# Performance work log

Hardware: AMD Instinct MI355X
Metric: run time of the kernel (lower is better)

Reference implementation:

```python
import jax, jax.numpy as jnp
import numpy as np

N = 50000
E = 600000
IN_C = 128
HID_C = 128
OUT_C = 128


def _glorot(key, shape):
    fan_in, fan_out = shape[0], shape[1]
    lim = np.sqrt(6.0 / (fan_in + fan_out))
    return jax.random.uniform(key, shape, jnp.float32, -lim, lim)


def setup_inputs() -> dict:
    key = jax.random.key(0)
    ks = jax.random.split(key, 10)
    x = jax.random.normal(ks[0], (N, IN_C), jnp.float32)
    edge_index = jax.random.randint(ks[1], (2, E), 0, N, jnp.int64)
    return {
        "x": x,
        "edge_index": edge_index,
        # SAGEConv1: lin_l (aggregated, with bias) and lin_r (root, no bias)
        "W1_l": _glorot(ks[2], (IN_C, HID_C)),
        "b1_l": jnp.zeros((HID_C,), jnp.float32),
        "W1_r": _glorot(ks[3], (IN_C, HID_C)),
        # SAGEConv2
        "W2_l": _glorot(ks[4], (HID_C, OUT_C)),
        "b2_l": jnp.zeros((OUT_C,), jnp.float32),
        "W2_r": _glorot(ks[5], (HID_C, OUT_C)),
        # final Linear(hidden+out -> out)
        "W_lin": _glorot(ks[6], (HID_C + OUT_C, OUT_C)),
        "b_lin": jnp.zeros((OUT_C,), jnp.float32),
    }


def _sage_conv(x, src, dst, W_l, b_l, W_r):
    # mean-aggregate source features onto destination nodes
    msg = x[src]                                   # [E, C] gather
    agg = jax.ops.segment_sum(msg, dst, num_segments=N)        # [N, C]
    cnt = jax.ops.segment_sum(jnp.ones((src.shape[0],), x.dtype), dst,
                              num_segments=N)                   # [N]
    mean = agg / jnp.maximum(cnt, 1.0)[:, None]
    return mean @ W_l + b_l + x @ W_r


def reference(x, edge_index, W1_l, b1_l, W1_r, W2_l, b2_l, W2_r, W_lin, b_lin):
    src, dst = edge_index[0], edge_index[1]
    x1 = jax.nn.relu(_sage_conv(x, src, dst, W1_l, b1_l, W1_r))   # [N, HID]
    x2 = jax.nn.relu(_sage_conv(x1, src, dst, W2_l, b2_l, W2_r))  # [N, OUT]
    return jnp.concatenate([x1, x2], axis=-1) @ W_lin + b_lin     # [N, OUT]
```

## Files before the change

kernel.cpp:

```cpp
#include <hip/hip_runtime.h>


typedef _Float16 f16;
typedef unsigned int u32;
typedef __attribute__((ext_vector_type(4))) _Float16 f16x4;
typedef __attribute__((ext_vector_type(8))) _Float16 f16x8;
typedef __attribute__((ext_vector_type(4))) float f32x4;

#define RNB 128

__global__ void prep_kernel(const float* __restrict__ x, f16* __restrict__ xh, int n4,
                            const int* __restrict__ ei, int* __restrict__ ghist, int E,
                            const float* __restrict__ W1l, const float* __restrict__ W1r,
                            const float* __restrict__ W2l, const float* __restrict__ W2r,
                            const float* __restrict__ Wlin, f16* __restrict__ wt,
                            int cb, int wb) {
  int b = blockIdx.x;
  if (b < cb) {
    int i = b * 256 + threadIdx.x;
    if (i < n4) {
      const float4 v = ((const float4*)x)[i];
      f16x4 h = { (f16)v.x, (f16)v.y, (f16)v.z, (f16)v.w };
      ((f16x4*)xh)[i] = h;
    }
  } else if (b < cb + wb) {
    int tid = (b - cb) * 256 + threadIdx.x;
    int w = tid >> 15, idx = tid & 32767;
    int j = idx & 7, n = (idx >> 3) & 127, chunk = idx >> 10;
    int k = chunk * 8 + j;
    float v;
    if (w == 0) v = (k < 128) ? W1l[k * 128 + n] : W1r[(k - 128) * 128 + n];
    else if (w == 1) v = (k < 128) ? W2l[k * 128 + n] : W2r[(k - 128) * 128 + n];
    else v = Wlin[k * 128 + n];
    wt[tid] = (f16)v;
  } else {
    __shared__ int h[256];
    int tid = threadIdx.x, rb = b - cb - wb;
    h[tid] = 0;
    __syncthreads();
    int per = (E + RNB - 1) / RNB;
    int s = rb * per, e = s + per; if (e > E) e = E;
    for (int i = s + tid; i < e; i += 256) atomicAdd(&h[ei[E + i] >> 8], 1);
    __syncthreads();
    ghist[tid * RNB + rb] = h[tid];
  }
}

__device__ inline int block_excl_scan256(int v, int* ws) {
  int lane = threadIdx.x & 63, w = threadIdx.x >> 6;
  int incl = v;
#pragma unroll
  for (int o = 1; o < 64; o <<= 1) {
    int u = __shfl_up(incl, o);
    if (lane >= o) incl += u;
  }
  if (lane == 63) ws[w] = incl;
  __syncthreads();
  int base = 0;
#pragma unroll
  for (int i = 0; i < 4; ++i) base += (i < w) ? ws[i] : 0;
  return base + incl - v;
}

__global__ void radix_scatter(const int* __restrict__ ei, const int* __restrict__ ghist,
                              u32* __restrict__ tmp, int E) {
  __shared__ int cur[256];
  __shared__ int ws[4];
  int tid = threadIdx.x, b = blockIdx.x;
  const int* row = ghist + tid * RNB;
  int part = 0, rest = 0;
  for (int i = 0; i < b; ++i) part += row[i];
  for (int i = b; i < RNB; ++i) rest += row[i];
  int total = part + rest;
  int excl = block_excl_scan256(total, ws);
  cur[tid] = excl + part;
  __syncthreads();
  int per = (E + RNB - 1) / RNB;
  int s = b * per, e = s + per; if (e > E) e = E;
  for (int i = s + tid; i < e; i += 256) {
    int d = ei[E + i], sr = ei[i];
    int pos = atomicAdd(&cur[d >> 8], 1);
    tmp[pos] = ((u32)sr << 8) | (u32)(d & 255);
  }
}

__global__ void radix_bucket(const u32* __restrict__ tmp, const int* __restrict__ ghist,
                             int* __restrict__ srcs, int* __restrict__ off,
                             int N, int E, int HB) {
  __shared__ int h[256], sc[256], cur[256];
  __shared__ int bsc[257];
  __shared__ int ws[4];
  int tid = threadIdx.x, hb = blockIdx.x;
  const int* row = ghist + tid * RNB;
  int total = 0;
#pragma unroll 4
  for (int i = 0; i < RNB; ++i) total += row[i];
  int excl = block_excl_scan256(total, ws);
  bsc[tid] = excl;
  if (tid == 255) bsc[256] = E;
  h[tid] = 0;
  __syncthreads();
  int start = bsc[hb];
  int end = bsc[hb + 1];
  for (int i = start + tid; i < end; i += 256) atomicAdd(&h[tmp[i] & 255u], 1);
  __syncthreads();
  sc[tid] = h[tid];
  __syncthreads();
  for (int o = 1; o < 256; o <<= 1) {
    int u = (tid >= o) ? sc[tid - o] : 0;
    __syncthreads();
    sc[tid] += u;
    __syncthreads();
  }
  int exclb = sc[tid] - h[tid];
  int v = (hb << 8) + tid;
  if (v < N) off[v] = start + exclb;
  if (hb == 0 && tid == 0) off[N] = E;
  cur[tid] = start + exclb;
  __syncthreads();
  for (int i = start + tid; i < end; i += 256) {
    u32 p = tmp[i];
    int pos = atomicAdd(&cur[p & 255u], 1);
    srcs[pos] = (int)(p >> 8);
  }
}

#define AGG_R 6
__global__ void aggregate_kernel(const f16* __restrict__ feat, const int* __restrict__ off,
                                 const int* __restrict__ srcs, f16* __restrict__ meanf, int n) {
  int pair = (int)((blockIdx.x * blockDim.x + threadIdx.x) >> 6);
  int w0 = pair * 2;
  if (w0 >= n) return;
  int w1 = w0 + 1;
  int lane = threadIdx.x & 63;
  int sub = lane >> 4, n15 = lane & 15;
  int beg0 = off[w0], end0 = off[w0 + 1];
  int beg1 = end0;
  int end1 = (w1 < n) ? off[w1 + 1] : end0;
  int deg0 = end0 - beg0, deg1 = end1 - beg1;

  int s0[AGG_R], s1[AGG_R];
  bool v0[AGG_R], v1[AGG_R];
#pragma unroll
  for (int k = 0; k < AGG_R; ++k) {
    int p = 4 * k + sub;
    v0[k] = p < deg0;  s0[k] = v0[k] ? srcs[beg0 + p] : 0;
    v1[k] = p < deg1;  s1[k] = v1[k] ? srcs[beg1 + p] : 0;
  }
  f16x8 g0[AGG_R], g1[AGG_R];
#pragma unroll
  for (int k = 0; k < AGG_R; ++k) {
    if (v0[k]) g0[k] = *(const f16x8*)(feat + (size_t)s0[k] * 128 + n15 * 8);
    if (v1[k]) g1[k] = *(const f16x8*)(feat + (size_t)s1[k] * 128 + n15 * 8);
  }
  float acc0[8] = {}, acc1[8] = {};
#pragma unroll
  for (int k = 0; k < AGG_R; ++k) {
    if (v0[k]) {
#pragma unroll
      for (int j = 0; j < 8; ++j) acc0[j] += (float)g0[k][j];
    }
    if (v1[k]) {
#pragma unroll
      for (int j = 0; j < 8; ++j) acc1[j] += (float)g1[k][j];
    }
  }
  for (int e = beg0 + 4 * AGG_R; e < end0; e += 4) {
    if (sub < end0 - e) {
      int s = srcs[e + sub];
      f16x8 g = *(const f16x8*)(feat + (size_t)s * 128 + n15 * 8);
#pragma unroll
      for (int j = 0; j < 8; ++j) acc0[j] += (float)g[j];
    }
  }
  for (int e = beg1 + 4 * AGG_R; e < end1; e += 4) {
    if (sub < end1 - e) {
      int s = srcs[e + sub];
      f16x8 g = *(const f16x8*)(feat + (size_t)s * 128 + n15 * 8);
#pragma unroll
      for (int j = 0; j < 8; ++j) acc1[j] += (float)g[j];
    }
  }
#pragma unroll
  for (int j = 0; j < 8; ++j) {
    acc0[j] += __shfl_xor(acc0[j], 16);
    acc0[j] += __shfl_xor(acc0[j], 32);
    acc1[j] += __shfl_xor(acc1[j], 16);
    acc1[j] += __shfl_xor(acc1[j], 32);
  }
  if (sub == 0) {
    float inv = 1.0f / fmaxf((float)deg0, 1.0f);
    f16x8 o;
#pragma unroll
    for (int j = 0; j < 8; ++j) o[j] = (f16)(acc0[j] * inv);
    *(f16x8*)(meanf + (size_t)w0 * 128 + n15 * 8) = o;
  } else if (sub == 1 && w1 < n) {
    float inv = 1.0f / fmaxf((float)deg1, 1.0f);
    f16x8 o;
#pragma unroll
    for (int j = 0; j < 8; ++j) o[j] = (f16)(acc1[j] * inv);
    *(f16x8*)(meanf + (size_t)w1 * 128 + n15 * 8) = o;
  }
}

template <bool RELU, bool OUT16>
__global__ __launch_bounds__(256, 2) void gemm_kernel(
    const f16* __restrict__ U, const f16* __restrict__ V, const f16* __restrict__ Wt,
    const float* __restrict__ bias, void* __restrict__ outp, int M) {
  __shared__ f16 ldsb[32768];
  int tid = threadIdx.x;
  int wave = tid >> 6, lane = tid & 63;
  int quad = lane >> 4, n15 = lane & 15;
  int m0 = blockIdx.x * 128 + wave * 32;
  int kq = quad * 8;

  f16x8 a[2][8];
#pragma unroll
  for (int r = 0; r < 2; ++r) {
    int row = m0 + r * 16 + n15;
    int rowc = row < M ? row : M - 1;
    const f16* bu = U + (size_t)rowc * 128 + kq;
    const f16* bv = V + (size_t)rowc * 128 + kq;
#pragma unroll
    for (int kk = 0; kk < 4; ++kk) a[r][kk] = *(const f16x8*)(bu + kk * 32);
#pragma unroll
    for (int kk = 4; kk < 8; ++kk) a[r][kk] = *(const f16x8*)(bv + (kk - 4) * 32);
  }

#pragma unroll
  for (int it = 0; it < 16; ++it) {
    int idx = it * 256 + tid;
    ((f16x8*)ldsb)[idx] = ((const f16x8*)Wt)[idx];
  }
  __syncthreads();

  f32x4 acc[2][8] = {};
#pragma unroll
  for (int kk = 0; kk < 8; ++kk) {
#pragma unroll
    for (int t = 0; t < 8; ++t) {
      f16x8 b = ((const f16x8*)ldsb)[(kk * 4 + quad) * 128 + t * 16 + n15];
#pragma unroll
      for (int r = 0; r < 2; ++r)
        acc[r][t] = __builtin_amdgcn_mfma_f32_16x16x32_f16(a[r][kk], b, acc[r][t], 0, 0, 0);
    }
  }

  int rbase0 = m0 + quad * 4;
#pragma unroll
  for (int t = 0; t < 8; ++t) {
    float bv = bias[t * 16 + n15];
#pragma unroll
    for (int r = 0; r < 2; ++r) {
#pragma unroll
      for (int i = 0; i < 4; ++i) {
        int row = rbase0 + r * 16 + i;
        if (row < M) {
          float v = acc[r][t][i] + bv;
          if (RELU) v = fmaxf(v, 0.f);
          size_t idx = (size_t)row * 128 + t * 16 + n15;
          if (OUT16) ((f16*)outp)[idx] = (f16)v;
          else       ((float*)outp)[idx] = v;
        }
      }
    }
  }
}

__global__ __launch_bounds__(256, 2) void gemm23_kernel(
    const f16* __restrict__ U,
    const f16* __restrict__ V,
    const f16* __restrict__ Wt2, const f16* __restrict__ Wt3,
    const float* __restrict__ b2, const float* __restrict__ b3,
    float* __restrict__ out, int M) {
  __shared__ f16 ldsb[32768];
  int tid = threadIdx.x;
  int wave = tid >> 6, lane = tid & 63;
  int quad = lane >> 4, n15 = lane & 15;
  int m0 = blockIdx.x * 128 + wave * 32;
  int kq = quad * 8;

  f16x8 a[2][8];
#pragma unroll
  for (int r = 0; r < 2; ++r) {
    int row = m0 + r * 16 + n15;
    int rowc = row < M ? row : M - 1;
    const f16* bu = U + (size_t)rowc * 128 + kq;
    const f16* bv = V + (size_t)rowc * 128 + kq;
#pragma unroll
    for (int kk = 0; kk < 4; ++kk) a[r][kk] = *(const f16x8*)(bu + kk * 32);
#pragma unroll
    for (int kk = 4; kk < 8; ++kk) a[r][kk] = *(const f16x8*)(bv + (kk - 4) * 32);
  }

#pragma unroll
  for (int it = 0; it < 16; ++it) {
    int idx = it * 256 + tid;
    ((f16x8*)ldsb)[idx] = ((const f16x8*)Wt2)[idx];
  }
  __syncthreads();

  f32x4 acc[2][8] = {};
#pragma unroll
  for (int kk = 0; kk < 8; ++kk) {
#pragma unroll
    for (int t = 0; t < 8; ++t) {
      f16x8 b = ((const f16x8*)ldsb)[(kk * 4 + quad) * 128 + t * 16 + n15];
#pragma unroll
      for (int r = 0; r < 2; ++r)
        acc[r][t] = __builtin_amdgcn_mfma_f32_16x16x32_f16(a[r][kk], b, acc[r][t], 0, 0, 0);
    }
  }

  __syncthreads();

#pragma unroll
  for (int t = 0; t < 8; ++t) {
    float bv = b2[t * 16 + n15];
    int chunk = t * 2 + (n15 >> 3);
    int offc = n15 & 7;
#pragma unroll
    for (int r = 0; r < 2; ++r) {
#pragma unroll
      for (int i = 0; i < 4; ++i) {
        int rowl = wave * 32 + r * 16 + quad * 4 + i;
        float v = fmaxf(acc[r][t][i] + bv, 0.f);
        ldsb[rowl * 128 + (((chunk ^ (rowl & 15)) << 3) | offc)] = (f16)v;
      }
    }
  }
  __syncthreads();

  f16x8 a2[2][4];
#pragma unroll
  for (int r = 0; r < 2; ++r) {
    int rowl = wave * 32 + r * 16 + n15;
#pragma unroll
    for (int kk2 = 0; kk2 < 4; ++kk2) {
      int chunk = kk2 * 4 + quad;
      a2[r][kk2] = *(const f16x8*)(ldsb + rowl * 128 + ((chunk ^ (rowl & 15)) << 3));
    }
  }

  f32x4 acc3[2][8] = {};
#pragma unroll
  for (int kk = 0; kk < 8; ++kk) {
#pragma unroll
    for (int t = 0; t < 8; ++t) {
      f16x8 b = ((const f16x8*)Wt3)[(kk * 4 + quad) * 128 + t * 16 + n15];
#pragma unroll
      for (int r = 0; r < 2; ++r) {
        f16x8 av = (kk < 4) ? a[r][4 + kk] : a2[r][kk - 4];
        acc3[r][t] = __builtin_amdgcn_mfma_f32_16x16x32_f16(av, b, acc3[r][t], 0, 0, 0);
      }
    }
  }

  int rbase0 = m0 + quad * 4;
#pragma unroll
  for (int t = 0; t < 8; ++t) {
    float bv = b3[t * 16 + n15];
#pragma unroll
    for (int r = 0; r < 2; ++r) {
#pragma unroll
      for (int i = 0; i < 4; ++i) {
        int row = rbase0 + r * 16 + i;
        if (row < M)
          out[(size_t)row * 128 + t * 16 + n15] = acc3[r][t][i] + bv;
      }
    }
  }
}

extern "C" void kernel_launch(void* const* d_in, const int* in_sizes, int n_in,
                              void* d_out, int out_size, void* d_ws, size_t ws_size,
                              hipStream_t stream) {
  (void)n_in; (void)out_size; (void)ws_size;
  const float* x    = (const float*)d_in[0];
  const int*   ei   = (const int*)d_in[1];
  const float* W1l  = (const float*)d_in[2];
  const float* b1l  = (const float*)d_in[3];
  const float* W1r  = (const float*)d_in[4];
  const float* W2l  = (const float*)d_in[5];
  const float* b2l  = (const float*)d_in[6];
  const float* W2r  = (const float*)d_in[7];
  const float* Wlin = (const float*)d_in[8];
  const float* blin = (const float*)d_in[9];
  const int N = in_sizes[0] / 128;
  const int E = in_sizes[1] / 2;

  char* ws = (char*)d_ws;
  size_t o = 0;
  auto alloc = [&](size_t bytes) {
    char* p = ws + o;
    o = (o + bytes + 255) & ~(size_t)255;
    return p;
  };
  f16*  xh   = (f16*)alloc((size_t)N * 128 * 2);
  f16*  x1h  = (f16*)alloc((size_t)N * 128 * 2);
  f16*  mh   = (f16*)alloc((size_t)N * 128 * 2);
  f16*  wt   = (f16*)alloc((size_t)3 * 32768 * 2);
  int*  off  = (int*)alloc(((size_t)N + 1) * 4);
  int*  srcs = (int*)alloc((size_t)E * 4);
  u32*  tmp  = (u32*)alloc((size_t)E * 4);
  int*  ghist= (int*)alloc(256 * RNB * 4);
  f16* wt1 = wt, *wt2 = wt + 32768, *wt3 = wt + 65536;

  const int n4 = N * 128 / 4;
  const int cb = (n4 + 255) / 256;
  const int wb = (3 * 32768) / 256;
  const int HB = (N + 255) / 256;

  prep_kernel<<<cb + wb + RNB, 256, 0, stream>>>(x, xh, n4, ei, ghist, E,
                                                 W1l, W1r, W2l, W2r, Wlin, wt, cb, wb);
  radix_scatter<<<RNB, 256, 0, stream>>>(ei, ghist, tmp, E);
  radix_bucket<<<HB, 256, 0, stream>>>(tmp, ghist, srcs, off, N, E, HB);

  const int aggBlocks  = ((N + 1) / 2 + 3) / 4;
  const int gemmBlocks = (N + 127) / 128;

  aggregate_kernel<<<aggBlocks, 256, 0, stream>>>(xh, off, srcs, mh, N);
  gemm_kernel<true, true><<<gemmBlocks, 256, 0, stream>>>(mh, xh, wt1, b1l, x1h, N);
  aggregate_kernel<<<aggBlocks, 256, 0, stream>>>(x1h, off, srcs, mh, N);
  gemm23_kernel<<<gemmBlocks, 256, 0, stream>>>(mh, x1h, wt2, wt3, b2l, blin,
                                                (float*)d_out, N);
}
```

Before: 229.0 us.

## Fuse mean aggregation with SAGE linear layers into per-tile kernels

Replaces the separate aggregate and GEMM kernels with one kernel per layer. Each block aggregates 32 nodes' neighbor means into LDS and immediately runs the MFMA GEMM with weights streamed through LDS in quarter chunks. This removes the global round-trip of the mean buffer and two launches. In exchange the row tiles are smaller, there are extra barriers for weight chunk reloads, and each block reloads the full weight matrices, i.e. more weight traffic per row.

Measured after the change: 226.1 us. Within noise of the previous version (-1.3%).

```diff
diff --git a/kernel.cpp b/kernel.cpp
--- a/kernel.cpp
+++ b/kernel.cpp
@@ -126,247 +126,198 @@
 }
 
 #define AGG_R 6
-__global__ void aggregate_kernel(const f16* __restrict__ feat, const int* __restrict__ off,
-                                 const int* __restrict__ srcs, f16* __restrict__ meanf, int n) {
-  int pair = (int)((blockIdx.x * blockDim.x + threadIdx.x) >> 6);
-  int w0 = pair * 2;
-  if (w0 >= n) return;
-  int w1 = w0 + 1;
-  int lane = threadIdx.x & 63;
-  int sub = lane >> 4, n15 = lane & 15;
-  int beg0 = off[w0], end0 = off[w0 + 1];
-  int beg1 = end0;
-  int end1 = (w1 < n) ? off[w1 + 1] : end0;
-  int deg0 = end0 - beg0, deg1 = end1 - beg1;
-
-  int s0[AGG_R], s1[AGG_R];
-  bool v0[AGG_R], v1[AGG_R];
-#pragma unroll
-  for (int k = 0; k < AGG_R; ++k) {
-    int p = 4 * k + sub;
-    v0[k] = p < deg0;  s0[k] = v0[k] ? srcs[beg0 + p] : 0;
-    v1[k] = p < deg1;  s1[k] = v1[k] ? srcs[beg1 + p] : 0;
-  }
-  f16x8 g0[AGG_R], g1[AGG_R];
-#pragma unroll
-  for (int k = 0; k < AGG_R; ++k) {
-    if (v0[k]) g0[k] = *(const f16x8*)(feat + (size_t)s0[k] * 128 + n15 * 8);
-    if (v1[k]) g1[k] = *(const f16x8*)(feat + (size_t)s1[k] * 128 + n15 * 8);
-  }
-  float acc0[8] = {}, acc1[8] = {};
-#pragma unroll
-  for (int k = 0; k < AGG_R; ++k) {
-    if (v0[k]) {
-#pragma unroll
-      for (int j = 0; j < 8; ++j) acc0[j] += (float)g0[k][j];
-    }
-    if (v1[k]) {
-#pragma unroll
-      for (int j = 0; j < 8; ++j) acc1[j] += (float)g1[k][j];
-    }
-  }
-  for (int e = beg0 + 4 * AGG_R; e < end0; e += 4) {
-    if (sub < end0 - e) {
-      int s = srcs[e + sub];
-      f16x8 g = *(const f16x8*)(feat + (size_t)s * 128 + n15 * 8);
-#pragma unroll
-      for (int j = 0; j < 8; ++j) acc0[j] += (float)g[j];
-    }
-  }
-  for (int e = beg1 + 4 * AGG_R; e < end1; e += 4) {
-    if (sub < end1 - e) {
-      int s = srcs[e + sub];
-      f16x8 g = *(const f16x8*)(feat + (size_t)s * 128 + n15 * 8);
-#pragma unroll
-      for (int j = 0; j < 8; ++j) acc1[j] += (float)g[j];
-    }
-  }
-#pragma unroll
-  for (int j = 0; j < 8; ++j) {
-    acc0[j] += __shfl_xor(acc0[j], 16);
-    acc0[j] += __shfl_xor(acc0[j], 32);
-    acc1[j] += __shfl_xor(acc1[j], 16);
-    acc1[j] += __shfl_xor(acc1[j], 32);
-  }
-  if (sub == 0) {
-    float inv = 1.0f / fmaxf((float)deg0, 1.0f);
-    f16x8 o;
-#pragma unroll
-    for (int j = 0; j < 8; ++j) o[j] = (f16)(acc0[j] * inv);
-    *(f16x8*)(meanf + (size_t)w0 * 128 + n15 * 8) = o;
-  } else if (sub == 1 && w1 < n) {
-    float inv = 1.0f / fmaxf((float)deg1, 1.0f);
-    f16x8 o;
-#pragma unroll
-    for (int j = 0; j < 8; ++j) o[j] = (f16)(acc1[j] * inv);
-    *(f16x8*)(meanf + (size_t)w1 * 128 + n15 * 8) = o;
-  }
-}
-
-template <bool RELU, bool OUT16>
-__global__ __launch_bounds__(256, 2) void gemm_kernel(
-    const f16* __restrict__ U, const f16* __restrict__ V, const f16* __restrict__ Wt,
-    const float* __restrict__ bias, void* __restrict__ outp, int M) {
-  __shared__ f16 ldsb[32768];
+template <bool HEAD>
+__global__ __launch_bounds__(256, 4) void fused_kernel(
+    const f16* __restrict__ feat,
+    const int* __restrict__ off, const int* __restrict__ srcs,
+    const f16* __restrict__ WtA, const f16* __restrict__ WtB,
+    const float* __restrict__ bA, const float* __restrict__ bB,
+    void* __restrict__ outp, int n) {
+  __shared__ f16 lds[16384];
   int tid = threadIdx.x;
   int wave = tid >> 6, lane = tid & 63;
-  int quad = lane >> 4, n15 = lane & 15;
-  int m0 = blockIdx.x * 128 + wave * 32;
-  int kq = quad * 8;
-
-  f16x8 a[2][8];
-#pragma unroll
-  for (int r = 0; r < 2; ++r) {
-    int row = m0 + r * 16 + n15;
-    int rowc = row < M ? row : M - 1;
-    const f16* bu = U + (size_t)rowc * 128 + kq;
-    const f16* bv = V + (size_t)rowc * 128 + kq;
-#pragma unroll
-    for (int kk = 0; kk < 4; ++kk) a[r][kk] = *(const f16x8*)(bu + kk * 32);
-#pragma unroll
-    for (int kk = 4; kk < 8; ++kk) a[r][kk] = *(const f16x8*)(bv + (kk - 4) * 32);
-  }
-
-#pragma unroll
-  for (int it = 0; it < 16; ++it) {
-    int idx = it * 256 + tid;
-    ((f16x8*)ldsb)[idx] = ((const f16x8*)Wt)[idx];
-  }
-  __syncthreads();
-
-  f32x4 acc[2][8] = {};
-#pragma unroll
-  for (int kk = 0; kk < 8; ++kk) {
-#pragma unroll
-    for (int t = 0; t < 8; ++t) {
-      f16x8 b = ((const f16x8*)ldsb)[(kk * 4 + quad) * 128 + t * 16 + n15];
-#pragma unroll
-      for (int r = 0; r < 2; ++r)
-        acc[r][t] = __builtin_amdgcn_mfma_f32_16x16x32_f16(a[r][kk], b, acc[r][t], 0, 0, 0);
-    }
-  }
-
-  int rbase0 = m0 + quad * 4;
-#pragma unroll
-  for (int t = 0; t < 8; ++t) {
-    float bv = bias[t * 16 + n15];
-#pragma unroll
-    for (int r = 0; r < 2; ++r) {
+  int sub = lane >> 4, n15 = lane & 15;
+  int base = blockIdx.x * 32;
+
+#pragma unroll
+  for (int i = 0; i < 4; ++i)
+    ((f16x8*)lds)[i * 256 + tid] = ((const f16x8*)WtA)[i * 256 + tid];
+
+#pragma unroll 1
+  for (int p = 0; p < 4; ++p) {
+    int ln0 = p * 8 + wave * 2;
+    int w0 = base + ln0, w1 = w0 + 1;
+    bool a0 = w0 < n, a1 = w1 < n;
+    int beg0 = a0 ? off[w0] : 0;
+    int end0 = a0 ? off[w0 + 1] : 0;
+    int beg1 = end0;
+    int end1 = a1 ? off[w1 + 1] : end0;
+    int deg0 = end0 - beg0, deg1 = end1 - beg1;
+
+    int s0[AGG_R], s1[AGG_R];
+    bool v0[AGG_R], v1[AGG_R];
+#pragma unroll
+    for (int k = 0; k < AGG_R; ++k) {
+      int pp = 4 * k + sub;
+      v0[k] = pp < deg0;  s0[k] = v0[k] ? srcs[beg0 + pp] : 0;
+      v1[k] = pp < deg1;  s1[k] = v1[k] ? srcs[beg1 + pp] : 0;
+    }
+    f16x8 g0[AGG_R], g1[AGG_R];
+#pragma unroll
+    for (int k = 0; k < AGG_R; ++k) {
+      if (v0[k]) g0[k] = *(const f16x8*)(feat + (size_t)s0[k] * 128 + n15 * 8);
+      if (v1[k]) g1[k] = *(const f16x8*)(feat + (size_t)s1[k] * 128 + n15 * 8);
+    }
+    float acc0[8] = {}, acc1[8] = {};
+#pragma unroll
+    for (int k = 0; k < AGG_R; ++k) {
+      if (v0[k]) {
+#pragma unroll
+        for (int j = 0; j < 8; ++j) acc0[j] += (float)g0[k][j];
+      }
+      if (v1[k]) {
+#pragma unroll
+        for (int j = 0; j < 8; ++j) acc1[j] += (float)g1[k][j];
+      }
+    }
+    for (int e = beg0 + 4 * AGG_R; e < end0; e += 4) {
+      if (sub < end0 - e) {
+        int s = srcs[e + sub];
+        f16x8 g = *(const f16x8*)(feat + (size_t)s * 128 + n15 * 8);
+#pragma unroll
+        for (int j = 0; j < 8; ++j) acc0[j] += (float)g[j];
+      }
+    }
+    for (int e = beg1 + 4 * AGG_R; e < end1; e += 4) {
+      if (sub < end1 - e) {
+        int s = srcs[e + sub];
+        f16x8 g = *(const f16x8*)(feat + (size_t)s * 128 + n15 * 8);
+#pragma unroll
+        for (int j = 0; j < 8; ++j) acc1[j] += (float)g[j];
+      }
+    }
+#pragma unroll
+    for (int j = 0; j < 8; ++j) {
+      acc0[j] += __shfl_xor(acc0[j], 16);
+      acc0[j] += __shfl_xor(acc0[j], 32);
+      acc1[j] += __shfl_xor(acc1[j], 16);
+      acc1[j] += __shfl_xor(acc1[j], 32);
+    }
+    if (sub == 0) {
+      float inv = 1.0f / fmaxf((float)deg0, 1.0f);
+      f16x8 o;
+#pragma unroll
+      for (int j = 0; j < 8; ++j) o[j] = (f16)(acc0[j] * inv);
+      *(f16x8*)(lds + 8192 + ln0 * 128 + ((n15 ^ (ln0 & 15)) << 3)) = o;
+    } else if (sub == 1) {
+      float inv = 1.0f / fmaxf((float)deg1, 1.0f);
+      int ln1 = ln0 + 1;
+      f16x8 o;
+#pragma unroll
+      for (int j = 0; j < 8; ++j) o[j] = (f16)(acc1[j] * inv);
+      *(f16x8*)(lds + 8192 + ln1 * 128 + ((n15 ^ (ln1 & 15)) << 3)) = o;
+    }
+  }
+  __syncthreads();
+
+  int rg = wave & 1, ch = wave >> 1;
+  int rowl = rg * 16 + n15;
+  int colb = ch * 64;
+
+  f16x8 a[8];
+#pragma unroll
+  for (int kk = 0; kk < 4; ++kk)
+    a[kk] = *(const f16x8*)(lds + 8192 + rowl * 128 + (((kk * 4 + sub) ^ n15) << 3));
+  {
+    int node = base + rowl; if (node >= n) node = n - 1;
+    const f16* bp = feat + (size_t)node * 128 + sub * 8;
+#pragma unroll
+    for (int kk = 4; kk < 8; ++kk) a[kk] = *(const f16x8*)(bp + (kk - 4) * 32);
+  }
+
+  f32x4 acc[4] = {};
+#pragma unroll
+  for (int q = 0; q < 4; ++q) {
+#pragma unroll
+    for (int kk = 2 * q; kk < 2 * q + 2; ++kk)
+#pragma unroll
+      for (int t = 0; t < 4; ++t) {
+        f16x8 bfr = ((const f16x8*)lds)[((kk * 4 + sub) & 7) * 128 + colb + t * 16 + n15];
+        acc[t] = __builtin_amdgcn_mfma_f32_16x16x32_f16(a[kk], bfr, acc[t], 0, 0, 0);
+      }
+    if (q < 3) {
+      __syncthreads();
+#pragma unroll
+      for (int i = 0; i < 4; ++i)
+        ((f16x8*)lds)[i * 256 + tid] = ((const f16x8*)WtA)[(q + 1) * 1024 + i * 256 + tid];
+      __syncthreads();
+    }
+  }
+
+  if (!HEAD) {
+#pragma unroll
+    for (int t = 0; t < 4; ++t) {
+      float bv = bA[colb + t * 16 + n15];
 #pragma unroll
       for (int i = 0; i < 4; ++i) {
-        int row = rbase0 + r * 16 + i;
-        if (row < M) {
-          float v = acc[r][t][i] + bv;
-          if (RELU) v = fmaxf(v, 0.f);
-          size_t idx = (size_t)row * 128 + t * 16 + n15;
-          if (OUT16) ((f16*)outp)[idx] = (f16)v;
-          else       ((float*)outp)[idx] = v;
+        int row = base + rg * 16 + sub * 4 + i;
+        if (row < n) {
+          float v = fmaxf(acc[t][i] + bv, 0.f);
+          ((f16*)outp)[(size_t)row * 128 + colb + t * 16 + n15] = (f16)v;
         }
       }
     }
-  }
-}
-
-__global__ __launch_bounds__(256, 2) void gemm23_kernel(
-    const f16* __restrict__ U,
-    const f16* __restrict__ V,
-    const f16* __restrict__ Wt2, const f16* __restrict__ Wt3,
-    const float* __restrict__ b2, const float* __restrict__ b3,
-    float* __restrict__ out, int M) {
-  __shared__ f16 ldsb[32768];
-  int tid = threadIdx.x;
-  int wave = tid >> 6, lane = tid & 63;
-  int quad = lane >> 4, n15 = lane & 15;
-  int m0 = blockIdx.x * 128 + wave * 32;
-  int kq = quad * 8;
-
-  f16x8 a[2][8];
-#pragma unroll
-  for (int r = 0; r < 2; ++r) {
-    int row = m0 + r * 16 + n15;
-    int rowc = row < M ? row : M - 1;
-    const f16* bu = U + (size_t)rowc * 128 + kq;
-    const f16* bv = V + (size_t)rowc * 128 + kq;
-#pragma unroll
-    for (int kk = 0; kk < 4; ++kk) a[r][kk] = *(const f16x8*)(bu + kk * 32);
-#pragma unroll
-    for (int kk = 4; kk < 8; ++kk) a[r][kk] = *(const f16x8*)(bv + (kk - 4) * 32);
-  }
-
-#pragma unroll
-  for (int it = 0; it < 16; ++it) {
-    int idx = it * 256 + tid;
-    ((f16x8*)ldsb)[idx] = ((const f16x8*)Wt2)[idx];
-  }
-  __syncthreads();
-
-  f32x4 acc[2][8] = {};
-#pragma unroll
-  for (int kk = 0; kk < 8; ++kk) {
-#pragma unroll
-    for (int t = 0; t < 8; ++t) {
-      f16x8 b = ((const f16x8*)ldsb)[(kk * 4 + quad) * 128 + t * 16 + n15];
-#pragma unroll
-      for (int r = 0; r < 2; ++r)
-        acc[r][t] = __builtin_amdgcn_mfma_f32_16x16x32_f16(a[r][kk], b, acc[r][t], 0, 0, 0);
-    }
-  }
-
-  __syncthreads();
-
-#pragma unroll
-  for (int t = 0; t < 8; ++t) {
-    float bv = b2[t * 16 + n15];
-    int chunk = t * 2 + (n15 >> 3);
-    int offc = n15 & 7;
-#pragma unroll
-    for (int r = 0; r < 2; ++r) {
+  } else {
+    __syncthreads();
+#pragma unroll
+    for (int t = 0; t < 4; ++t) {
+      float bv = bA[colb + t * 16 + n15];
+      int col = colb + t * 16 + n15;
+      int cchunk = col >> 3, coff = col & 7;
 #pragma unroll
       for (int i = 0; i < 4; ++i) {
-        int rowl = wave * 32 + r * 16 + quad * 4 + i;
-        float v = fmaxf(acc[r][t][i] + bv, 0.f);
-        ldsb[rowl * 128 + (((chunk ^ (rowl & 15)) << 3) | offc)] = (f16)v;
-      }
-    }
-  }
-  __syncthreads();
-
-  f16x8 a2[2][4];
-#pragma unroll
-  for (int r = 0; r < 2; ++r) {
-    int rowl = wave * 32 + r * 16 + n15;
-#pragma unroll
-    for (int kk2 = 0; kk2 < 4; ++kk2) {
-      int chunk = kk2 * 4 + quad;
-      a2[r][kk2] = *(const f16x8*)(ldsb + rowl * 128 + ((chunk ^ (rowl & 15)) << 3));
-    }
-  }
-
-  f32x4 acc3[2][8] = {};
-#pragma unroll
-  for (int kk = 0; kk < 8; ++kk) {
-#pragma unroll
-    for (int t = 0; t < 8; ++t) {
-      f16x8 b = ((const f16x8*)Wt3)[(kk * 4 + quad) * 128 + t * 16 + n15];
-#pragma unroll
-      for (int r = 0; r < 2; ++r) {
-        f16x8 av = (kk < 4) ? a[r][4 + kk] : a2[r][kk - 4];
-        acc3[r][t] = __builtin_amdgcn_mfma_f32_16x16x32_f16(av, b, acc3[r][t], 0, 0, 0);
-      }
-    }
-  }
-
-  int rbase0 = m0 + quad * 4;
-#pragma unroll
-  for (int t = 0; t < 8; ++t) {
-    float bv = b3[t * 16 + n15];
-#pragma unroll
-    for (int r = 0; r < 2; ++r) {
+        int rw = rg * 16 + sub * 4 + i;
+        float v = fmaxf(acc[t][i] + bv, 0.f);
+        lds[12288 + rw * 128 + (((cchunk ^ (rw & 15)) << 3) | coff)] = (f16)v;
+      }
+    }
+#pragma unroll
+    for (int i = 0; i < 4; ++i)
+      ((f16x8*)lds)[i * 256 + tid] = ((const f16x8*)WtB)[i * 256 + tid];
+    __syncthreads();
+
+    f16x8 a2[4];
+#pragma unroll
+    for (int kk2 = 0; kk2 < 4; ++kk2)
+      a2[kk2] = *(const f16x8*)(lds + 12288 + rowl * 128 + (((kk2 * 4 + sub) ^ n15) << 3));
+
+    f32x4 acc3[4] = {};
+#pragma unroll
+    for (int q = 0; q < 4; ++q) {
+#pragma unroll
+      for (int kk = 2 * q; kk < 2 * q + 2; ++kk)
+#pragma unroll
+        for (int t = 0; t < 4; ++t) {
+          f16x8 bfr = ((const f16x8*)lds)[((kk * 4 + sub) & 7) * 128 + colb + t * 16 + n15];
+          f16x8 av = (kk < 4) ? a[4 + kk] : a2[kk - 4];
+          acc3[t] = __builtin_amdgcn_mfma_f32_16x16x32_f16(av, bfr, acc3[t], 0, 0, 0);
+        }
+      if (q < 3) {
+        __syncthreads();
+#pragma unroll
+        for (int i = 0; i < 4; ++i)
+          ((f16x8*)lds)[i * 256 + tid] = ((const f16x8*)WtB)[(q + 1) * 1024 + i * 256 + tid];
+        __syncthreads();
+      }
+    }
+#pragma unroll
+    for (int t = 0; t < 4; ++t) {
+      float bv = bB[colb + t * 16 + n15];
 #pragma unroll
       for (int i = 0; i < 4; ++i) {
-        int row = rbase0 + r * 16 + i;
-        if (row < M)
-          out[(size_t)row * 128 + t * 16 + n15] = acc3[r][t][i] + bv;
+        int row = base + rg * 16 + sub * 4 + i;
+        if (row < n)
+          ((float*)outp)[(size_t)row * 128 + colb + t * 16 + n15] = acc3[t][i] + bv;
       }
     }
   }
@@ -398,7 +349,6 @@
   };
   f16*  xh   = (f16*)alloc((size_t)N * 128 * 2);
   f16*  x1h  = (f16*)alloc((size_t)N * 128 * 2);
-  f16*  mh   = (f16*)alloc((size_t)N * 128 * 2);
   f16*  wt   = (f16*)alloc((size_t)3 * 32768 * 2);
   int*  off  = (int*)alloc(((size_t)N + 1) * 4);
   int*  srcs = (int*)alloc((size_t)E * 4);
@@ -416,12 +366,10 @@
   radix_scatter<<<RNB, 256, 0, stream>>>(ei, ghist, tmp, E);
   radix_bucket<<<HB, 256, 0, stream>>>(tmp, ghist, srcs, off, N, E, HB);
 
-  const int aggBlocks  = ((N + 1) / 2 + 3) / 4;
-  const int gemmBlocks = (N + 127) / 128;
-
-  aggregate_kernel<<<aggBlocks, 256, 0, stream>>>(xh, off, srcs, mh, N);
-  gemm_kernel<true, true><<<gemmBlocks, 256, 0, stream>>>(mh, xh, wt1, b1l, x1h, N);
-  aggregate_kernel<<<aggBlocks, 256, 0, stream>>>(x1h, off, srcs, mh, N);
-  gemm23_kernel<<<gemmBlocks, 256, 0, stream>>>(mh, x1h, wt2, wt3, b2l, blin,
-                                                (float*)d_out, N);
-}
+  const int fusedBlocks = (N + 31) / 32;
+
+  fused_kernel<false><<<fusedBlocks, 256, 0, stream>>>(
+      xh, off, srcs, wt1, (const f16*)nullptr, b1l, (const float*)nullptr, x1h, N);
+  fused_kernel<true><<<fusedBlocks, 256, 0, stream>>>(
+      x1h, off, srcs, wt2, wt3, b2l, blin, d_out, N);
+}
```
